# Optimization experiments

Hardware: AMD Instinct MI355X
Metric: run time of the kernel (lower is better)

Reference implementation:

```python
import jax, jax.numpy as jnp
import numpy as np

N = 20000       # nodes
E = 320000      # edges (without self-loops)
D_IN = 256
HID = 64        # per-head channels, layer 1
HEADS = 4
D_OUT = 256
EPS = 1e-5      # LayerNorm eps
SLOPE = 0.2     # LeakyReLU negative slope (PyG GATConv default)


def setup_inputs() -> dict:
    key = jax.random.key(0)
    ks = jax.random.split(key, 10)
    def glorot(k, shape):
        fan_in, fan_out = shape[0], int(np.prod(shape[1:]))
        s = np.sqrt(2.0 / (fan_in + fan_out)).astype(np.float32)
        return jax.random.normal(k, shape, dtype=jnp.float32) * s
    x = jax.random.normal(ks[0], (N, D_IN), dtype=jnp.float32)
    edge_index = jax.random.randint(ks[1], (2, E), 0, N, dtype=jnp.int64)
    return {
        "x": x,
        "edge_index": edge_index,
        # layer 1: GATConv(D_IN, HID, heads=4, concat=True)
        "W1": glorot(ks[2], (D_IN, HEADS * HID)),
        "a1_src": glorot(ks[3], (HEADS, HID)),
        "a1_dst": glorot(ks[4], (HEADS, HID)),
        "b1": jnp.zeros((HEADS * HID,), jnp.float32),
        # LayerNorm(HEADS*HID)
        "ln_g": jnp.ones((HEADS * HID,), jnp.float32),
        "ln_b": jnp.zeros((HEADS * HID,), jnp.float32),
        # layer 2: GATConv(HEADS*HID, D_OUT, heads=1, concat=False)
        "W2": glorot(ks[5], (HEADS * HID, D_OUT)),
        "a2_src": glorot(ks[6], (1, D_OUT)),
        "a2_dst": glorot(ks[7], (1, D_OUT)),
        "b2": jnp.zeros((D_OUT,), jnp.float32),
    }


def _gat(x, src, dst, W, a_src, a_dst, b, heads, ch, concat):
    """PyG-style GATConv (self-loops already appended to src/dst)."""
    n = x.shape[0]
    h = (x @ W).reshape(n, heads, ch)                      # [n,H,C]
    es = (h * a_src).sum(-1)                               # [n,H] src logits
    ed = (h * a_dst).sum(-1)                               # [n,H] dst logits
    e = jax.nn.leaky_relu(es[src] + ed[dst], SLOPE)        # [Etot,H]
    # softmax over incoming edges of each dst node (stable)
    m = jax.ops.segment_max(e, dst, num_segments=n)
    w = jnp.exp(e - m[dst])
    den = jax.ops.segment_sum(w, dst, num_segments=n)
    alpha = w / den[dst]                                   # [Etot,H]
    msg = h[src] * alpha[:, :, None]                       # [Etot,H,C]
    out = jax.ops.segment_sum(msg, dst, num_segments=n)    # [n,H,C]
    out = out.reshape(n, heads * ch) if concat else out.mean(axis=1)
    return out + b


def _layernorm(x, g, b):
    mu = x.mean(-1, keepdims=True)
    v = ((x - mu) ** 2).mean(-1, keepdims=True)
    return (x - mu) * jax.lax.rsqrt(v + EPS) * g + b


def reference(x, edge_index, W1, a1_src, a1_dst, b1, ln_g, ln_b, W2, a2_src, a2_dst, b2):
    loops = jnp.arange(N, dtype=edge_index.dtype)
    src = jnp.concatenate([edge_index[0], loops])
    dst = jnp.concatenate([edge_index[1], loops])
    h = _gat(x, src, dst, W1, a1_src, a1_dst, b1, HEADS, HID, True)
    h = jax.nn.relu(_layernorm(h, ln_g, ln_b))             # dropout is identity in eval
    out = _gat(h, src, dst, W2, a2_src, a2_dst, b2, 1, D_OUT, False)
    return out
```

## Files before the change

### kernel.cpp

```cpp
#include <hip/hip_runtime.h>
#include <hip/hip_bf16.h>
#include <math.h>

#define N_NODES 20000
#define N_EDGES 320000
#define N_ETOT  (N_EDGES + N_NODES)
#define SLOPE 0.2f
#define LN_EPS 1e-5f

typedef __attribute__((ext_vector_type(8))) short short8v;
typedef __attribute__((ext_vector_type(4))) float f32x4;

__device__ __forceinline__ float lrelu(float x) { return x > 0.f ? x : SLOPE * x; }

__device__ __forceinline__ float rlf(float v, int l) {
  return __uint_as_float(__builtin_amdgcn_readlane(__float_as_uint(v), l));
}
__device__ __forceinline__ int rli(int v, int l) { return __builtin_amdgcn_readlane(v, l); }

__device__ __forceinline__ unsigned short f2bf(float f) {
  __hip_bfloat16 h = __float2bfloat16(f);
  return *reinterpret_cast<unsigned short*>(&h);
}
__device__ __forceinline__ float bf2f(unsigned short u) {
  return __uint_as_float(((unsigned int)u) << 16);
}

__global__ __launch_bounds__(256) void k_count(const int* __restrict__ ei, int* __restrict__ cnt) {
  int i = blockIdx.x * 256 + threadIdx.x;
  if (i >= N_ETOT) return;
  int d = (i < N_EDGES) ? ei[N_EDGES + i] : (i - N_EDGES);
  atomicAdd(&cnt[d], 1);
}

__global__ __launch_bounds__(1024) void k_scan(int* __restrict__ cnt, int* __restrict__ off) {
  __shared__ int wsum[16], wpref[16];
  __shared__ int base_s;
  int tid = threadIdx.x, lane = tid & 63, wid = tid >> 6;
  if (tid == 0) { base_s = 0; off[0] = 0; }
  __syncthreads();
  for (int c = 0; c < 20; ++c) {
    int i = c * 1024 + tid;
    int v = (i < N_NODES) ? cnt[i] : 0;
    if (i < N_NODES) cnt[i] = 0;
    int incl = v;
#pragma unroll
    for (int d = 1; d < 64; d <<= 1) { int t = __shfl_up(incl, d); if (lane >= d) incl += t; }
    if (lane == 63) wsum[wid] = incl;
    __syncthreads();
    if (wid == 0 && lane < 16) {
      int s = wsum[lane];
#pragma unroll
      for (int d = 1; d < 16; d <<= 1) { int t = __shfl_up(s, d); if (lane >= d) s += t; }
      wpref[lane] = s;
    }
    __syncthreads();
    int wbase = wid ? wpref[wid - 1] : 0;
    if (i < N_NODES) off[i + 1] = base_s + wbase + incl;
    __syncthreads();
    if (tid == 0) base_s += wpref[15];
    __syncthreads();
  }
}

__global__ __launch_bounds__(256) void k_scatter(const int* __restrict__ ei, const int* __restrict__ off,
                                                 int* __restrict__ cursor, int* __restrict__ srcs) {
  int i = blockIdx.x * 256 + threadIdx.x;
  if (i >= N_ETOT) return;
  int s, d;
  if (i < N_EDGES) { s = ei[i]; d = ei[N_EDGES + i]; } else { s = i - N_EDGES; d = s; }
  int pos = off[d] + atomicAdd(&cursor[d], 1);
  srcs[pos] = s;
}

__global__ __launch_bounds__(256) void k_prep(const float* __restrict__ W1, const float* __restrict__ W2,
                                              unsigned short* __restrict__ P1, unsigned short* __restrict__ P2) {
  int b = blockIdx.x, t = threadIdx.x;
  int e = (b & 255) * 256 + t;
  int j = e & 7, lane = (e >> 3) & 63, nf = (e >> 9) & 7, ks = (e >> 12) & 7, nh = (e >> 15) & 1;
  int col = nh * 128 + nf * 16 + (lane & 15);
  int k = ks * 32 + (lane >> 4) * 8 + j;
  if (b < 256) P1[e] = f2bf(W1[k * 256 + col]);
  else         P2[e] = f2bf(W2[k * 256 + col]);
}

template <int A_BF16, int HEADS>
__global__ __launch_bounds__(256) void k_mfma_gemm(const void* __restrict__ Av,
                                                   const unsigned short* __restrict__ Wp,
                                                   const float* __restrict__ asrc,
                                                   const float* __restrict__ adst,
                                                   unsigned short* __restrict__ C,
                                                   float* __restrict__ es, float* __restrict__ ed) {
  int gwave = blockIdx.x * 4 + (threadIdx.x >> 6);
  int wtile = gwave >> 1;
  int nhalf = gwave & 1;
  int lane = threadIdx.x & 63;
  int r = lane & 15, kg = lane >> 4;
  int rbase = wtile * 16;
  int cbase = nhalf * 128;

  f32x4 acc[8];
#pragma unroll
  for (int i = 0; i < 8; ++i) acc[i] = (f32x4){0.f, 0.f, 0.f, 0.f};

  const float* Af = (const float*)Av;
  const unsigned short* Ab = (const unsigned short*)Av;
  const unsigned short* Wb = Wp + nhalf * 32768;

#pragma unroll
  for (int ks = 0; ks < 8; ++ks) {
    int koff = ks * 32 + kg * 8;
    short8v a;
    if (A_BF16) {
      int4 raw = *reinterpret_cast<const int4*>(&Ab[(size_t)(rbase + r) * 256 + koff]);
      a = __builtin_bit_cast(short8v, raw);
    } else {
      float4 lo = *reinterpret_cast<const float4*>(&Af[(size_t)(rbase + r) * 256 + koff]);
      float4 hi = *reinterpret_cast<const float4*>(&Af[(size_t)(rbase + r) * 256 + koff + 4]);
      a[0] = (short)f2bf(lo.x); a[1] = (short)f2bf(lo.y); a[2] = (short)f2bf(lo.z); a[3] = (short)f2bf(lo.w);
      a[4] = (short)f2bf(hi.x); a[5] = (short)f2bf(hi.y); a[6] = (short)f2bf(hi.z); a[7] = (short)f2bf(hi.w);
    }
#pragma unroll
    for (int nf = 0; nf < 8; ++nf) {
      int4 braw = *reinterpret_cast<const int4*>(&Wb[(size_t)(ks * 8 + nf) * 512 + lane * 8]);
      short8v b = __builtin_bit_cast(short8v, braw);
      acc[nf] = __builtin_amdgcn_mfma_f32_16x16x32_bf16(a, b, acc[nf], 0, 0, 0);
    }
  }

#pragma unroll
  for (int nf = 0; nf < 8; ++nf) {
#pragma unroll
    for (int q = 0; q < 4; ++q) {
      int row = rbase + kg * 4 + q;
      int col = cbase + nf * 16 + r;
      C[(size_t)row * 256 + col] = f2bf(acc[nf][q]);
    }
  }

  float as_v[8], ad_v[8];
#pragma unroll
  for (int nf = 0; nf < 8; ++nf) {
    int col = cbase + nf * 16 + r;
    as_v[nf] = asrc[col];
    ad_v[nf] = adst[col];
  }
  if (HEADS == 4) {
#pragma unroll
    for (int q = 0; q < 4; ++q) {
      float s0 = 0.f, s1 = 0.f, d0 = 0.f, d1 = 0.f;
#pragma unroll
      for (int nf = 0; nf < 4; ++nf) {
        s0 = fmaf(acc[nf][q], as_v[nf], s0);
        d0 = fmaf(acc[nf][q], ad_v[nf], d0);
        s1 = fmaf(acc[nf + 4][q], as_v[nf + 4], s1);
        d1 = fmaf(acc[nf + 4][q], ad_v[nf + 4], d1);
      }
#pragma unroll
      for (int s = 1; s < 16; s <<= 1) {
        s0 += __shfl_xor(s0, s); s1 += __shfl_xor(s1, s);
        d0 += __shfl_xor(d0, s); d1 += __shfl_xor(d1, s);
      }
      if (r == 0) {
        int row = rbase + kg * 4 + q;
        int hl = nhalf * 2;
        atomicAdd(&es[row * 4 + hl], s0);
        atomicAdd(&es[row * 4 + hl + 1], s1);
        atomicAdd(&ed[row * 4 + hl], d0);
        atomicAdd(&ed[row * 4 + hl + 1], d1);
      }
    }
  } else {
#pragma unroll
    for (int q = 0; q < 4; ++q) {
      float s0 = 0.f, d0 = 0.f;
#pragma unroll
      for (int nf = 0; nf < 8; ++nf) {
        s0 = fmaf(acc[nf][q], as_v[nf], s0);
        d0 = fmaf(acc[nf][q], ad_v[nf], d0);
      }
#pragma unroll
      for (int s = 1; s < 16; s <<= 1) {
        s0 += __shfl_xor(s0, s);
        d0 += __shfl_xor(d0, s);
      }
      if (r == 0) {
        int row = rbase + kg * 4 + q;
        atomicAdd(&es[row], s0);
        atomicAdd(&ed[row], d0);
      }
    }
  }
}

__global__ __launch_bounds__(256) void k_gat1_ln(const unsigned short* __restrict__ h1,
                                                 const float* __restrict__ es, const float* __restrict__ ed,
                                                 const int* __restrict__ off, const int* __restrict__ srcs,
                                                 const float* __restrict__ b1, const float* __restrict__ lng,
                                                 const float* __restrict__ lnb, unsigned short* __restrict__ hmid) {
  int n = (blockIdx.x * 256 + threadIdx.x) >> 6;
  if (n >= N_NODES) return;
  int lane = threadIdx.x & 63;
  int myh = lane >> 4;
  int beg = off[n], end = off[n + 1], deg = end - beg;
  float4 edv = *reinterpret_cast<const float4*>(&ed[n * 4]);
  float ax = 0.f, ay = 0.f, az = 0.f, aw = 0.f;
  float invden;

  if (deg <= 64) {
    int sv = 0;
    float e0 = -1e30f, e1 = -1e30f, e2 = -1e30f, e3 = -1e30f;
    bool valid = lane < deg;
    if (valid) {
      sv = srcs[beg + lane];
      float4 esv = *reinterpret_cast<const float4*>(&es[sv * 4]);
      e0 = lrelu(esv.x + edv.x); e1 = lrelu(esv.y + edv.y);
      e2 = lrelu(esv.z + edv.z); e3 = lrelu(esv.w + edv.w);
    }
    float m0 = e0, m1 = e1, m2 = e2, m3 = e3;
#pragma unroll
    for (int s = 1; s < 64; s <<= 1) {
      m0 = fmaxf(m0, __shfl_xor(m0, s)); m1 = fmaxf(m1, __shfl_xor(m1, s));
      m2 = fmaxf(m2, __shfl_xor(m2, s)); m3 = fmaxf(m3, __shfl_xor(m3, s));
    }
    float w0 = valid ? __expf(e0 - m0) : 0.f;
    float w1 = valid ? __expf(e1 - m1) : 0.f;
    float w2 = valid ? __expf(e2 - m2) : 0.f;
    float w3 = valid ? __expf(e3 - m3) : 0.f;
    float d0 = w0, d1 = w1, d2 = w2, d3 = w3;
#pragma unroll
    for (int s = 1; s < 64; s <<= 1) {
      d0 += __shfl_xor(d0, s); d1 += __shfl_xor(d1, s);
      d2 += __shfl_xor(d2, s); d3 += __shfl_xor(d3, s);
    }
    float den = (myh == 0) ? d0 : (myh == 1) ? d1 : (myh == 2) ? d2 : d3;
    invden = 1.f / den;

    int j = 0;
    for (; j + 4 <= deg; j += 4) {
      int s0 = rli(sv, j), s1 = rli(sv, j + 1), s2 = rli(sv, j + 2), s3 = rli(sv, j + 3);
      ushort4 v0 = *reinterpret_cast<const ushort4*>(&h1[(size_t)s0 * 256 + lane * 4]);
      ushort4 v1 = *reinterpret_cast<const ushort4*>(&h1[(size_t)s1 * 256 + lane * 4]);
      ushort4 v2 = *reinterpret_cast<const ushort4*>(&h1[(size_t)s2 * 256 + lane * 4]);
      ushort4 v3 = *reinterpret_cast<const ushort4*>(&h1[(size_t)s3 * 256 + lane * 4]);
#pragma unroll
      for (int q = 0; q < 4; ++q) {
        int jj = j + q;
        float w0j = rlf(w0, jj), w1j = rlf(w1, jj), w2j = rlf(w2, jj), w3j = rlf(w3, jj);
        float wj = (myh == 0) ? w0j : (myh == 1) ? w1j : (myh == 2) ? w2j : w3j;
        ushort4 v = (q == 0) ? v0 : (q == 1) ? v1 : (q == 2) ? v2 : v3;
        ax = fmaf(wj, bf2f(v.x), ax); ay = fmaf(wj, bf2f(v.y), ay);
        az = fmaf(wj, bf2f(v.z), az); aw = fmaf(wj, bf2f(v.w), aw);
      }
    }
    for (; j < deg; ++j) {
      int sj = rli(sv, j);
      float w0j = rlf(w0, j), w1j = rlf(w1, j), w2j = rlf(w2, j), w3j = rlf(w3, j);
      float wj = (myh == 0) ? w0j : (myh == 1) ? w1j : (myh == 2) ? w2j : w3j;
      ushort4 v = *reinterpret_cast<const ushort4*>(&h1[(size_t)sj * 256 + lane * 4]);
      ax = fmaf(wj, bf2f(v.x), ax); ay = fmaf(wj, bf2f(v.y), ay);
      az = fmaf(wj, bf2f(v.z), az); aw = fmaf(wj, bf2f(v.w), aw);
    }
  } else {
    float m0 = -1e30f, m1 = -1e30f, m2 = -1e30f, m3 = -1e30f;
    for (int j = beg + lane; j < end; j += 64) {
      int s = srcs[j];
      float4 esv = *reinterpret_cast<const float4*>(&es[s * 4]);
      m0 = fmaxf(m0, lrelu(esv.x + edv.x)); m1 = fmaxf(m1, lrelu(esv.y + edv.y));
      m2 = fmaxf(m2, lrelu(esv.z + edv.z)); m3 = fmaxf(m3, lrelu(esv.w + edv.w));
    }
#pragma unroll
    for (int s = 1; s < 64; s <<= 1) {
      m0 = fmaxf(m0, __shfl_xor(m0, s)); m1 = fmaxf(m1, __shfl_xor(m1, s));
      m2 = fmaxf(m2, __shfl_xor(m2, s)); m3 = fmaxf(m3, __shfl_xor(m3, s));
    }
    float edh = (myh == 0) ? edv.x : (myh == 1) ? edv.y : (myh == 2) ? edv.z : edv.w;
    float mh = (myh == 0) ? m0 : (myh == 1) ? m1 : (myh == 2) ? m2 : m3;
    float den = 0.f;
    for (int j = beg; j < end; ++j) {
      int s = srcs[j];
      float e = lrelu(es[s * 4 + myh] + edh);
      float w = __expf(e - mh);
      den += w;
      ushort4 v = *reinterpret_cast<const ushort4*>(&h1[(size_t)s * 256 + lane * 4]);
      ax = fmaf(w, bf2f(v.x), ax); ay = fmaf(w, bf2f(v.y), ay);
      az = fmaf(w, bf2f(v.z), az); aw = fmaf(w, bf2f(v.w), aw);
    }
    invden = 1.f / den;
  }

  float4 bb = *reinterpret_cast<const float4*>(&b1[lane * 4]);
  float vx = ax * invden + bb.x, vy = ay * invden + bb.y;
  float vz = az * invden + bb.z, vw = aw * invden + bb.w;
  float sum = vx + vy + vz + vw;
  float sq = vx * vx + vy * vy + vz * vz + vw * vw;
#pragma unroll
  for (int s = 1; s < 64; s <<= 1) { sum += __shfl_xor(sum, s); sq += __shfl_xor(sq, s); }
  float mu = sum * (1.f / 256.f);
  float var = sq * (1.f / 256.f) - mu * mu;
  float rstd = rsqrtf(var + LN_EPS);
  float4 g = *reinterpret_cast<const float4*>(&lng[lane * 4]);
  float4 lb = *reinterpret_cast<const float4*>(&lnb[lane * 4]);
  ushort4 o;
  o.x = f2bf(fmaxf(0.f, (vx - mu) * rstd * g.x + lb.x));
  o.y = f2bf(fmaxf(0.f, (vy - mu) * rstd * g.y + lb.y));
  o.z = f2bf(fmaxf(0.f, (vz - mu) * rstd * g.z + lb.z));
  o.w = f2bf(fmaxf(0.f, (vw - mu) * rstd * g.w + lb.w));
  *reinterpret_cast<ushort4*>(&hmid[(size_t)n * 256 + lane * 4]) = o;
}

__global__ __launch_bounds__(256) void k_gat2(const unsigned short* __restrict__ h2,
                                              const float* __restrict__ es, const float* __restrict__ ed,
                                              const int* __restrict__ off, const int* __restrict__ srcs,
                                              const float* __restrict__ b2, float* __restrict__ out) {
  int n = (blockIdx.x * 256 + threadIdx.x) >> 6;
  if (n >= N_NODES) return;
  int lane = threadIdx.x & 63;
  int beg = off[n], end = off[n + 1], deg = end - beg;
  float edn = ed[n];
  float ax = 0.f, ay = 0.f, az = 0.f, aw = 0.f;
  float invden;

  if (deg <= 64) {
    int sv = 0;
    float e = -1e30f;
    bool valid = lane < deg;
    if (valid) {
      sv = srcs[beg + lane];
      e = lrelu(es[sv] + edn);
    }
    float m = e;
#pragma unroll
    for (int s = 1; s < 64; s <<= 1) m = fmaxf(m, __shfl_xor(m, s));
    float wv = valid ? __expf(e - m) : 0.f;
    float den = wv;
#pragma unroll
    for (int s = 1; s < 64; s <<= 1) den += __shfl_xor(den, s);
    invden = 1.f / den;

    int j = 0;
    for (; j + 4 <= deg; j += 4) {
      int s0 = rli(sv, j), s1 = rli(sv, j + 1), s2 = rli(sv, j + 2), s3 = rli(sv, j + 3);
      ushort4 v0 = *reinterpret_cast<const ushort4*>(&h2[(size_t)s0 * 256 + lane * 4]);
      ushort4 v1 = *reinterpret_cast<const ushort4*>(&h2[(size_t)s1 * 256 + lane * 4]);
      ushort4 v2 = *reinterpret_cast<const ushort4*>(&h2[(size_t)s2 * 256 + lane * 4]);
      ushort4 v3 = *reinterpret_cast<const ushort4*>(&h2[(size_t)s3 * 256 + lane * 4]);
      float wj0 = rlf(wv, j), wj1 = rlf(wv, j + 1), wj2 = rlf(wv, j + 2), wj3 = rlf(wv, j + 3);
      ax = fmaf(wj0, bf2f(v0.x), ax); ay = fmaf(wj0, bf2f(v0.y), ay);
      az = fmaf(wj0, bf2f(v0.z), az); aw = fmaf(wj0, bf2f(v0.w), aw);
      ax = fmaf(wj1, bf2f(v1.x), ax); ay = fmaf(wj1, bf2f(v1.y), ay);
      az = fmaf(wj1, bf2f(v1.z), az); aw = fmaf(wj1, bf2f(v1.w), aw);
      ax = fmaf(wj2, bf2f(v2.x), ax); ay = fmaf(wj2, bf2f(v2.y), ay);
      az = fmaf(wj2, bf2f(v2.z), az); aw = fmaf(wj2, bf2f(v2.w), aw);
      ax = fmaf(wj3, bf2f(v3.x), ax); ay = fmaf(wj3, bf2f(v3.y), ay);
      az = fmaf(wj3, bf2f(v3.z), az); aw = fmaf(wj3, bf2f(v3.w), aw);
    }
    for (; j < deg; ++j) {
      int sj = rli(sv, j);
      float wj = rlf(wv, j);
      ushort4 v = *reinterpret_cast<const ushort4*>(&h2[(size_t)sj * 256 + lane * 4]);
      ax = fmaf(wj, bf2f(v.x), ax); ay = fmaf(wj, bf2f(v.y), ay);
      az = fmaf(wj, bf2f(v.z), az); aw = fmaf(wj, bf2f(v.w), aw);
    }
  } else {
    float m = -1e30f;
    for (int j = beg + lane; j < end; j += 64) m = fmaxf(m, lrelu(es[srcs[j]] + edn));
#pragma unroll
    for (int s = 1; s < 64; s <<= 1) m = fmaxf(m, __shfl_xor(m, s));
    float den = 0.f;
    for (int j = beg; j < end; ++j) {
      int s = srcs[j];
      float w = __expf(lrelu(es[s] + edn) - m);
      den += w;
      ushort4 v = *reinterpret_cast<const ushort4*>(&h2[(size_t)s * 256 + lane * 4]);
      ax = fmaf(w, bf2f(v.x), ax); ay = fmaf(w, bf2f(v.y), ay);
      az = fmaf(w, bf2f(v.z), az); aw = fmaf(w, bf2f(v.w), aw);
    }
    invden = 1.f / den;
  }

  float4 bb = *reinterpret_cast<const float4*>(&b2[lane * 4]);
  float4 o = make_float4(ax * invden + bb.x, ay * invden + bb.y, az * invden + bb.z, aw * invden + bb.w);
  *reinterpret_cast<float4*>(&out[(size_t)n * 256 + lane * 4]) = o;
}

extern "C" void kernel_launch(void* const* d_in, const int* in_sizes, int n_in,
                              void* d_out, int out_size, void* d_ws, size_t ws_size,
                              hipStream_t stream) {
  (void)in_sizes; (void)n_in; (void)out_size; (void)ws_size;
  const float* x   = (const float*)d_in[0];
  const int*   ei  = (const int*)d_in[1];
  const float* W1  = (const float*)d_in[2];
  const float* a1s = (const float*)d_in[3];
  const float* a1d = (const float*)d_in[4];
  const float* b1  = (const float*)d_in[5];
  const float* lng = (const float*)d_in[6];
  const float* lnb = (const float*)d_in[7];
  const float* W2  = (const float*)d_in[8];
  const float* a2s = (const float*)d_in[9];
  const float* a2d = (const float*)d_in[10];
  const float* b2  = (const float*)d_in[11];
  float* out = (float*)d_out;

  char* ws = (char*)d_ws;
  unsigned short* h1b   = (unsigned short*)(ws + 0);
  unsigned short* hmidb = (unsigned short*)(ws + 10240000);
  unsigned short* h2b   = (unsigned short*)(ws + 20480000);
  unsigned short* Wp1   = (unsigned short*)(ws + 30720000);
  unsigned short* Wp2   = (unsigned short*)(ws + 30851072);
  float* es1 = (float*)(ws + 30982144);
  float* ed1 = (float*)(ws + 31302144);
  float* es2 = (float*)(ws + 31622144);
  float* ed2 = (float*)(ws + 31702144);
  int*   off = (int*)(ws + 31782144);
  int*   cnt = (int*)(ws + 31862148);
  int*   srcs = (int*)(ws + 31942148);

  hipMemsetAsync(cnt, 0, N_NODES * sizeof(int), stream);
  hipMemsetAsync(es1, 0, 800000, stream);

  k_count<<<(N_ETOT + 255) / 256, 256, 0, stream>>>(ei, cnt);
  k_scan<<<1, 1024, 0, stream>>>(cnt, off);
  k_scatter<<<(N_ETOT + 255) / 256, 256, 0, stream>>>(ei, off, cnt, srcs);

  k_prep<<<512, 256, 0, stream>>>(W1, W2, Wp1, Wp2);

  k_mfma_gemm<0, 4><<<625, 256, 0, stream>>>((const void*)x, Wp1, a1s, a1d, h1b, es1, ed1);
  k_gat1_ln<<<(N_NODES * 64) / 256, 256, 0, stream>>>(h1b, es1, ed1, off, srcs, b1, lng, lnb, hmidb);

  k_mfma_gemm<1, 1><<<625, 256, 0, stream>>>((const void*)hmidb, Wp2, a2s, a2d, h2b, es2, ed2);
  k_gat2<<<(N_NODES * 64) / 256, 256, 0, stream>>>(h2b, es2, ed2, off, srcs, b2, out);
}
```

Baseline: 232.8 us.

## Fuse CSR build and weight packing into one persistent kernel with grid barriers

Replaces the two memsets and the count, single-block scan, scatter and weight-prep kernels with one 256-block persistent kernel that uses atomic grid-wide barriers between phases. The scan becomes a two-level multi-block scan instead of a serial 1024-thread loop. The goal is to cut launch overhead and the slow single-block scan. In exchange it relies on all 256 blocks being co-resident for the spin barrier, and it keeps a small memset to reset the barrier counter.

```diff
diff --git a/kernel.cpp b/kernel.cpp
--- a/kernel.cpp
+++ b/kernel.cpp
@@ -7,6 +7,8 @@
 #define N_ETOT  (N_EDGES + N_NODES)
 #define SLOPE 0.2f
 #define LN_EPS 1e-5f
+#define NBLK 256
+#define NTHR 65536
 
 typedef __attribute__((ext_vector_type(8))) short short8v;
 typedef __attribute__((ext_vector_type(4))) float f32x4;
@@ -26,62 +28,102 @@
   return __uint_as_float(((unsigned int)u) << 16);
 }
 
-__global__ __launch_bounds__(256) void k_count(const int* __restrict__ ei, int* __restrict__ cnt) {
-  int i = blockIdx.x * 256 + threadIdx.x;
-  if (i >= N_ETOT) return;
-  int d = (i < N_EDGES) ? ei[N_EDGES + i] : (i - N_EDGES);
-  atomicAdd(&cnt[d], 1);
-}
-
-__global__ __launch_bounds__(1024) void k_scan(int* __restrict__ cnt, int* __restrict__ off) {
-  __shared__ int wsum[16], wpref[16];
-  __shared__ int base_s;
-  int tid = threadIdx.x, lane = tid & 63, wid = tid >> 6;
-  if (tid == 0) { base_s = 0; off[0] = 0; }
+__device__ __forceinline__ int aload(const int* p) {
+  return __hip_atomic_load(p, __ATOMIC_RELAXED, __HIP_MEMORY_SCOPE_AGENT);
+}
+__device__ __forceinline__ void astore(int* p, int v) {
+  __hip_atomic_store(p, v, __ATOMIC_RELAXED, __HIP_MEMORY_SCOPE_AGENT);
+}
+
+__device__ __forceinline__ void gbar(unsigned* bar, unsigned target) {
+  __threadfence();
   __syncthreads();
-  for (int c = 0; c < 20; ++c) {
-    int i = c * 1024 + tid;
-    int v = (i < N_NODES) ? cnt[i] : 0;
-    if (i < N_NODES) cnt[i] = 0;
-    int incl = v;
-#pragma unroll
-    for (int d = 1; d < 64; d <<= 1) { int t = __shfl_up(incl, d); if (lane >= d) incl += t; }
-    if (lane == 63) wsum[wid] = incl;
-    __syncthreads();
-    if (wid == 0 && lane < 16) {
-      int s = wsum[lane];
-#pragma unroll
-      for (int d = 1; d < 16; d <<= 1) { int t = __shfl_up(s, d); if (lane >= d) s += t; }
-      wpref[lane] = s;
-    }
-    __syncthreads();
-    int wbase = wid ? wpref[wid - 1] : 0;
-    if (i < N_NODES) off[i + 1] = base_s + wbase + incl;
-    __syncthreads();
-    if (tid == 0) base_s += wpref[15];
-    __syncthreads();
-  }
-}
-
-__global__ __launch_bounds__(256) void k_scatter(const int* __restrict__ ei, const int* __restrict__ off,
-                                                 int* __restrict__ cursor, int* __restrict__ srcs) {
-  int i = blockIdx.x * 256 + threadIdx.x;
-  if (i >= N_ETOT) return;
-  int s, d;
-  if (i < N_EDGES) { s = ei[i]; d = ei[N_EDGES + i]; } else { s = i - N_EDGES; d = s; }
-  int pos = off[d] + atomicAdd(&cursor[d], 1);
-  srcs[pos] = s;
-}
-
-__global__ __launch_bounds__(256) void k_prep(const float* __restrict__ W1, const float* __restrict__ W2,
-                                              unsigned short* __restrict__ P1, unsigned short* __restrict__ P2) {
-  int b = blockIdx.x, t = threadIdx.x;
-  int e = (b & 255) * 256 + t;
-  int j = e & 7, lane = (e >> 3) & 63, nf = (e >> 9) & 7, ks = (e >> 12) & 7, nh = (e >> 15) & 1;
-  int col = nh * 128 + nf * 16 + (lane & 15);
-  int k = ks * 32 + (lane >> 4) * 8 + j;
-  if (b < 256) P1[e] = f2bf(W1[k * 256 + col]);
-  else         P2[e] = f2bf(W2[k * 256 + col]);
+  if (threadIdx.x == 0) {
+    __hip_atomic_fetch_add(bar, 1u, __ATOMIC_RELEASE, __HIP_MEMORY_SCOPE_AGENT);
+    while (__hip_atomic_load(bar, __ATOMIC_ACQUIRE, __HIP_MEMORY_SCOPE_AGENT) < target)
+      __builtin_amdgcn_s_sleep(4);
+  }
+  __syncthreads();
+  __threadfence();
+}
+
+__device__ __forceinline__ int blockScan(int val, int tid, int* ldsw, int* total) {
+  int lane = tid & 63, w = tid >> 6;
+  int incl = val;
+#pragma unroll
+  for (int d = 1; d < 64; d <<= 1) { int t = __shfl_up(incl, d); if (lane >= d) incl += t; }
+  if (lane == 63) ldsw[w] = incl;
+  __syncthreads();
+  if (w == 0 && lane < 4) {
+    int s = ldsw[lane];
+#pragma unroll
+    for (int d = 1; d < 4; d <<= 1) { int t = __shfl_up(s, d); if (lane >= d) s += t; }
+    ldsw[lane] = s;
+  }
+  __syncthreads();
+  if (w > 0) incl += ldsw[w - 1];
+  *total = ldsw[3];
+  return incl;
+}
+
+__global__ __launch_bounds__(256) void k_graph(const int* __restrict__ ei,
+                                               const float* __restrict__ W1, const float* __restrict__ W2,
+                                               unsigned short* __restrict__ P1w, unsigned short* __restrict__ P2w,
+                                               int* __restrict__ cnt, int* __restrict__ off,
+                                               int* __restrict__ srcs, float* __restrict__ eszero,
+                                               int* __restrict__ bsum, unsigned* __restrict__ bar) {
+  __shared__ int ldsw[4];
+  int tid = threadIdx.x;
+  int b = blockIdx.x;
+  int g = b * 256 + tid;
+
+  if (g < N_NODES) cnt[g] = 0;
+  {
+    float4* z = (float4*)eszero;
+    if (g < 50000) z[g] = make_float4(0.f, 0.f, 0.f, 0.f);
+    int e = g;
+    int j = e & 7, lane = (e >> 3) & 63, nf = (e >> 9) & 7, ks = (e >> 12) & 7, nh = (e >> 15) & 1;
+    int col = nh * 128 + nf * 16 + (lane & 15);
+    int k = ks * 32 + (lane >> 4) * 8 + j;
+    P1w[e] = f2bf(W1[k * 256 + col]);
+    P2w[e] = f2bf(W2[k * 256 + col]);
+  }
+  gbar(bar, 256u);
+
+  for (int i = g; i < N_ETOT; i += NTHR) {
+    int d = (i < N_EDGES) ? ei[N_EDGES + i] : (i - N_EDGES);
+    atomicAdd(&cnt[d], 1);
+  }
+  gbar(bar, 512u);
+
+  int val = (g < N_NODES) ? aload(&cnt[g]) : 0;
+  int tot;
+  int incl = blockScan(val, tid, ldsw, &tot);
+  if (tid == 0) astore(&bsum[b], tot);
+  gbar(bar, 768u);
+
+  if (b == 0) {
+    int v = aload(&bsum[tid]);
+    int t2;
+    int inc2 = blockScan(v, tid, ldsw, &t2);
+    astore(&bsum[tid], inc2);
+  }
+  gbar(bar, 1024u);
+
+  int base = b ? aload(&bsum[b - 1]) : 0;
+  if (g < N_NODES) {
+    off[g + 1] = base + incl;
+    astore(&cnt[g], 0);
+  }
+  if (g == 0) off[0] = 0;
+  gbar(bar, 1280u);
+
+  for (int i = g; i < N_ETOT; i += NTHR) {
+    int s, d;
+    if (i < N_EDGES) { s = ei[i]; d = ei[N_EDGES + i]; } else { s = i - N_EDGES; d = s; }
+    int pos = aload(&off[d]) + atomicAdd(&cnt[d], 1);
+    srcs[pos] = s;
+  }
 }
 
 template <int A_BF16, int HEADS>
@@ -415,15 +457,12 @@
   int*   off = (int*)(ws + 31782144);
   int*   cnt = (int*)(ws + 31862148);
   int*   srcs = (int*)(ws + 31942148);
-
-  hipMemsetAsync(cnt, 0, N_NODES * sizeof(int), stream);
-  hipMemsetAsync(es1, 0, 800000, stream);
-
-  k_count<<<(N_ETOT + 255) / 256, 256, 0, stream>>>(ei, cnt);
-  k_scan<<<1, 1024, 0, stream>>>(cnt, off);
-  k_scatter<<<(N_ETOT + 255) / 256, 256, 0, stream>>>(ei, off, cnt, srcs);
-
-  k_prep<<<512, 256, 0, stream>>>(W1, W2, Wp1, Wp2);
+  unsigned* bar = (unsigned*)(ws + 33302148);
+  int*   bsum = (int*)(ws + 33302160);
+
+  hipMemsetAsync(bar, 0, 8, stream);
+
+  k_graph<<<NBLK, 256, 0, stream>>>(ei, W1, W2, Wp1, Wp2, cnt, off, srcs, es1, bsum, bar);
 
   k_mfma_gemm<0, 4><<<625, 256, 0, stream>>>((const void*)x, Wp1, a1s, a1d, h1b, es1, ed1);
   k_gat1_ln<<<(N_NODES * 64) / 256, 256, 0, stream>>>(h1b, es1, ed1, off, srcs, b1, lng, lnb, hmidb);
```

New measurement: 419.0 us. +80.0%, slower.

## Parallelize CSR scan, fuse count with weight prep, widen GEMM waves to full rows

Applied to the files above, without the earlier changes.

The single-block serial scan over 20 chunks becomes a two-kernel multi-block scan: per-block scan, then an add of the block-sum prefix. Edge counting and weight packing are merged into one launch, and the memset for es1/ed1 is dropped. Each GEMM wave now covers all 256 output columns for its 16 rows, so attention logits are written directly instead of combined with float atomics across two column halves. This cuts launch count, serialization and atomics, but doubles accumulator registers per wave and halves the number of waves, which may lower occupancy.

```diff
diff --git a/kernel.cpp b/kernel.cpp
--- a/kernel.cpp
+++ b/kernel.cpp
@@ -7,6 +7,7 @@
 #define N_ETOT  (N_EDGES + N_NODES)
 #define SLOPE 0.2f
 #define LN_EPS 1e-5f
+#define CNT_BLOCKS 1329
 
 typedef __attribute__((ext_vector_type(8))) short short8v;
 typedef __attribute__((ext_vector_type(4))) float f32x4;
@@ -26,41 +27,77 @@
   return __uint_as_float(((unsigned int)u) << 16);
 }
 
-__global__ __launch_bounds__(256) void k_count(const int* __restrict__ ei, int* __restrict__ cnt) {
-  int i = blockIdx.x * 256 + threadIdx.x;
-  if (i >= N_ETOT) return;
-  int d = (i < N_EDGES) ? ei[N_EDGES + i] : (i - N_EDGES);
-  atomicAdd(&cnt[d], 1);
-}
-
-__global__ __launch_bounds__(1024) void k_scan(int* __restrict__ cnt, int* __restrict__ off) {
-  __shared__ int wsum[16], wpref[16];
-  __shared__ int base_s;
-  int tid = threadIdx.x, lane = tid & 63, wid = tid >> 6;
-  if (tid == 0) { base_s = 0; off[0] = 0; }
+__global__ __launch_bounds__(256) void k_count_prep(const int* __restrict__ ei, int* __restrict__ cnt,
+                                                    const float* __restrict__ W1, const float* __restrict__ W2,
+                                                    unsigned short* __restrict__ P1, unsigned short* __restrict__ P2) {
+  int b = blockIdx.x, tid = threadIdx.x;
+  if (b < CNT_BLOCKS) {
+    int i = b * 256 + tid;
+    if (i < N_ETOT) {
+      int d = (i < N_EDGES) ? ei[N_EDGES + i] : (i - N_EDGES);
+      atomicAdd(&cnt[d], 1);
+    }
+  } else {
+    int e = (b - CNT_BLOCKS) * 256 + tid;
+    int j = e & 7, lane = (e >> 3) & 63, nf = (e >> 9) & 15, ks = (e >> 13) & 7;
+    int col = nf * 16 + (lane & 15);
+    int k = ks * 32 + (lane >> 4) * 8 + j;
+    P1[e] = f2bf(W1[k * 256 + col]);
+    P2[e] = f2bf(W2[k * 256 + col]);
+  }
+}
+
+__device__ __forceinline__ int blockScan512(int val, int tid, int* ldsw, int* total) {
+  int lane = tid & 63, w = tid >> 6;
+  int incl = val;
+#pragma unroll
+  for (int d = 1; d < 64; d <<= 1) { int t = __shfl_up(incl, d); if (lane >= d) incl += t; }
+  if (lane == 63) ldsw[w] = incl;
   __syncthreads();
-  for (int c = 0; c < 20; ++c) {
-    int i = c * 1024 + tid;
-    int v = (i < N_NODES) ? cnt[i] : 0;
-    if (i < N_NODES) cnt[i] = 0;
-    int incl = v;
-#pragma unroll
-    for (int d = 1; d < 64; d <<= 1) { int t = __shfl_up(incl, d); if (lane >= d) incl += t; }
-    if (lane == 63) wsum[wid] = incl;
-    __syncthreads();
-    if (wid == 0 && lane < 16) {
-      int s = wsum[lane];
-#pragma unroll
-      for (int d = 1; d < 16; d <<= 1) { int t = __shfl_up(s, d); if (lane >= d) s += t; }
-      wpref[lane] = s;
-    }
-    __syncthreads();
-    int wbase = wid ? wpref[wid - 1] : 0;
-    if (i < N_NODES) off[i + 1] = base_s + wbase + incl;
-    __syncthreads();
-    if (tid == 0) base_s += wpref[15];
-    __syncthreads();
-  }
+  if (w == 0 && lane < 8) {
+    int s = ldsw[lane];
+#pragma unroll
+    for (int d = 1; d < 8; d <<= 1) { int t = __shfl_up(s, d); if (lane >= d) s += t; }
+    ldsw[lane] = s;
+  }
+  __syncthreads();
+  if (w > 0) incl += ldsw[w - 1];
+  *total = ldsw[7];
+  return incl;
+}
+
+__global__ __launch_bounds__(512) void k_scanA(const int* __restrict__ cnt, int* __restrict__ off,
+                                               int* __restrict__ bsum) {
+  __shared__ int ldsw[8];
+  int tid = threadIdx.x, b = blockIdx.x;
+  int g = b * 512 + tid;
+  int val = (g < N_NODES) ? cnt[g] : 0;
+  int tot;
+  int incl = blockScan512(val, tid, ldsw, &tot);
+  if (g < N_NODES) off[g + 1] = incl;
+  if (tid == 0) bsum[b] = tot;
+}
+
+__global__ __launch_bounds__(512) void k_scanB(int* __restrict__ off, const int* __restrict__ bsum,
+                                               int* __restrict__ cnt) {
+  __shared__ int sbase;
+  int tid = threadIdx.x, b = blockIdx.x;
+  if (tid < 64) {
+    int v = (tid < 40) ? bsum[tid] : 0;
+    int inc = v;
+#pragma unroll
+    for (int d = 1; d < 64; d <<= 1) { int t = __shfl_up(inc, d); if (tid >= d) inc += t; }
+    int base = (b == 0) ? 0 : rli(inc, b - 1);
+    if (tid == 0) sbase = base;
+  }
+  __syncthreads();
+  int base = sbase;
+  int g = b * 512 + tid;
+  if (g < N_NODES) {
+    off[g + 1] += base;
+    cnt[g] = 0;
+  }
+  if (g == 0) off[0] = 0;
 }
 
 __global__ __launch_bounds__(256) void k_scatter(const int* __restrict__ ei, const int* __restrict__ off,
@@ -73,39 +110,25 @@
   srcs[pos] = s;
 }
 
-__global__ __launch_bounds__(256) void k_prep(const float* __restrict__ W1, const float* __restrict__ W2,
-                                              unsigned short* __restrict__ P1, unsigned short* __restrict__ P2) {
-  int b = blockIdx.x, t = threadIdx.x;
-  int e = (b & 255) * 256 + t;
-  int j = e & 7, lane = (e >> 3) & 63, nf = (e >> 9) & 7, ks = (e >> 12) & 7, nh = (e >> 15) & 1;
-  int col = nh * 128 + nf * 16 + (lane & 15);
-  int k = ks * 32 + (lane >> 4) * 8 + j;
-  if (b < 256) P1[e] = f2bf(W1[k * 256 + col]);
-  else         P2[e] = f2bf(W2[k * 256 + col]);
-}
-
 template <int A_BF16, int HEADS>
-__global__ __launch_bounds__(256) void k_mfma_gemm(const void* __restrict__ Av,
-                                                   const unsigned short* __restrict__ Wp,
-                                                   const float* __restrict__ asrc,
-                                                   const float* __restrict__ adst,
-                                                   unsigned short* __restrict__ C,
-                                                   float* __restrict__ es, float* __restrict__ ed) {
+__global__ __launch_bounds__(256) void k_gemm(const void* __restrict__ Av,
+                                              const unsigned short* __restrict__ Wp,
+                                              const float* __restrict__ asrc,
+                                              const float* __restrict__ adst,
+                                              unsigned short* __restrict__ C,
+                                              float* __restrict__ es, float* __restrict__ ed) {
   int gwave = blockIdx.x * 4 + (threadIdx.x >> 6);
-  int wtile = gwave >> 1;
-  int nhalf = gwave & 1;
+  if (gwave >= 1250) return;
   int lane = threadIdx.x & 63;
   int r = lane & 15, kg = lane >> 4;
-  int rbase = wtile * 16;
-  int cbase = nhalf * 128;
-
-  f32x4 acc[8];
-#pragma unroll
-  for (int i = 0; i < 8; ++i) acc[i] = (f32x4){0.f, 0.f, 0.f, 0.f};
+  int rbase = gwave * 16;
+
+  f32x4 acc[16];
+#pragma unroll
+  for (int i = 0; i < 16; ++i) acc[i] = (f32x4){0.f, 0.f, 0.f, 0.f};
 
   const float* Af = (const float*)Av;
   const unsigned short* Ab = (const unsigned short*)Av;
-  const unsigned short* Wb = Wp + nhalf * 32768;
 
 #pragma unroll
   for (int ks = 0; ks < 8; ++ks) {
@@ -121,53 +144,53 @@
       a[4] = (short)f2bf(hi.x); a[5] = (short)f2bf(hi.y); a[6] = (short)f2bf(hi.z); a[7] = (short)f2bf(hi.w);
     }
 #pragma unroll
-    for (int nf = 0; nf < 8; ++nf) {
-      int4 braw = *reinterpret_cast<const int4*>(&Wb[(size_t)(ks * 8 + nf) * 512 + lane * 8]);
-      short8v b = __builtin_bit_cast(short8v, braw);
-      acc[nf] = __builtin_amdgcn_mfma_f32_16x16x32_bf16(a, b, acc[nf], 0, 0, 0);
-    }
-  }
-
-#pragma unroll
-  for (int nf = 0; nf < 8; ++nf) {
+    for (int nf = 0; nf < 16; ++nf) {
+      int4 braw = *reinterpret_cast<const int4*>(&Wp[(size_t)(ks * 16 + nf) * 512 + lane * 8]);
+      short8v bfr = __builtin_bit_cast(short8v, braw);
+      acc[nf] = __builtin_amdgcn_mfma_f32_16x16x32_bf16(a, bfr, acc[nf], 0, 0, 0);
+    }
+  }
+
+#pragma unroll
+  for (int nf = 0; nf < 16; ++nf) {
 #pragma unroll
     for (int q = 0; q < 4; ++q) {
-      int row = rbase + kg * 4 + q;
-      int col = cbase + nf * 16 + r;
-      C[(size_t)row * 256 + col] = f2bf(acc[nf][q]);
-    }
-  }
-
-  float as_v[8], ad_v[8];
-#pragma unroll
-  for (int nf = 0; nf < 8; ++nf) {
-    int col = cbase + nf * 16 + r;
-    as_v[nf] = asrc[col];
-    ad_v[nf] = adst[col];
+      C[(size_t)(rbase + kg * 4 + q) * 256 + nf * 16 + r] = f2bf(acc[nf][q]);
+    }
+  }
+
+  float as_v[16], ad_v[16];
+#pragma unroll
+  for (int nf = 0; nf < 16; ++nf) {
+    as_v[nf] = asrc[nf * 16 + r];
+    ad_v[nf] = adst[nf * 16 + r];
   }
   if (HEADS == 4) {
 #pragma unroll
     for (int q = 0; q < 4; ++q) {
-      float s0 = 0.f, s1 = 0.f, d0 = 0.f, d1 = 0.f;
-#pragma unroll
-      for (int nf = 0; nf < 4; ++nf) {
-        s0 = fmaf(acc[nf][q], as_v[nf], s0);
-        d0 = fmaf(acc[nf][q], ad_v[nf], d0);
-        s1 = fmaf(acc[nf + 4][q], as_v[nf + 4], s1);
-        d1 = fmaf(acc[nf + 4][q], ad_v[nf + 4], d1);
-      }
-#pragma unroll
-      for (int s = 1; s < 16; s <<= 1) {
-        s0 += __shfl_xor(s0, s); s1 += __shfl_xor(s1, s);
-        d0 += __shfl_xor(d0, s); d1 += __shfl_xor(d1, s);
+      float hs[4], hd[4];
+#pragma unroll
+      for (int h = 0; h < 4; ++h) {
+        hs[h] = 0.f; hd[h] = 0.f;
+#pragma unroll
+        for (int t = 0; t < 4; ++t) {
+          int nf = h * 4 + t;
+          hs[h] = fmaf(acc[nf][q], as_v[nf], hs[h]);
+          hd[h] = fmaf(acc[nf][q], ad_v[nf], hd[h]);
+        }
+#pragma unroll
+        for (int s = 1; s < 16; s <<= 1) {
+          hs[h] += __shfl_xor(hs[h], s);
+          hd[h] += __shfl_xor(hd[h], s);
+        }
       }
       if (r == 0) {
         int row = rbase + kg * 4 + q;
-        int hl = nhalf * 2;
-        atomicAdd(&es[row * 4 + hl], s0);
-        atomicAdd(&es[row * 4 + hl + 1], s1);
-        atomicAdd(&ed[row * 4 + hl], d0);
-        atomicAdd(&ed[row * 4 + hl + 1], d1);
+#pragma unroll
+        for (int h = 0; h < 4; ++h) {
+          es[row * 4 + h] = hs[h];
+          ed[row * 4 + h] = hd[h];
+        }
       }
     }
   } else {
@@ -175,7 +198,7 @@
     for (int q = 0; q < 4; ++q) {
       float s0 = 0.f, d0 = 0.f;
 #pragma unroll
-      for (int nf = 0; nf < 8; ++nf) {
+      for (int nf = 0; nf < 16; ++nf) {
         s0 = fmaf(acc[nf][q], as_v[nf], s0);
         d0 = fmaf(acc[nf][q], ad_v[nf], d0);
       }
@@ -186,8 +209,8 @@
       }
       if (r == 0) {
         int row = rbase + kg * 4 + q;
-        atomicAdd(&es[row], s0);
-        atomicAdd(&ed[row], d0);
+        es[row] = s0;
+        ed[row] = d0;
       }
     }
   }
@@ -415,19 +438,17 @@
   int*   off = (int*)(ws + 31782144);
   int*   cnt = (int*)(ws + 31862148);
   int*   srcs = (int*)(ws + 31942148);
+  int*   bsum = (int*)(ws + 33302160);
 
   hipMemsetAsync(cnt, 0, N_NODES * sizeof(int), stream);
-  hipMemsetAsync(es1, 0, 800000, stream);
-
-  k_count<<<(N_ETOT + 255) / 256, 256, 0, stream>>>(ei, cnt);
-  k_scan<<<1, 1024, 0, stream>>>(cnt, off);
-  k_scatter<<<(N_ETOT + 255) / 256, 256, 0, stream>>>(ei, off, cnt, srcs);
-
-  k_prep<<<512, 256, 0, stream>>>(W1, W2, Wp1, Wp2);
-
-  k_mfma_gemm<0, 4><<<625, 256, 0, stream>>>((const void*)x, Wp1, a1s, a1d, h1b, es1, ed1);
+  k_count_prep<<<CNT_BLOCKS + 256, 256, 0, stream>>>(ei, cnt, W1, W2, Wp1, Wp2);
+  k_scanA<<<40, 512, 0, stream>>>(cnt, off, bsum);
+  k_scanB<<<40, 512, 0, stream>>>(off, bsum, cnt);
+  k_scatter<<<CNT_BLOCKS, 256, 0, stream>>>(ei, off, cnt, srcs);
+
+  k_gemm<0, 4><<<313, 256, 0, stream>>>((const void*)x, Wp1, a1s, a1d, h1b, es1, ed1);
   k_gat1_ln<<<(N_NODES * 64) / 256, 256, 0, stream>>>(h1b, es1, ed1, off, srcs, b1, lng, lnb, hmidb);
 
-  k_mfma_gemm<1, 1><<<625, 256, 0, stream>>>((const void*)hmidb, Wp2, a2s, a2d, h2b, es2, ed2);
+  k_gemm<1, 1><<<313, 256, 0, stream>>>((const void*)hmidb, Wp2, a2s, a2d, h2b, es2, ed2);
   k_gat2<<<(N_NODES * 64) / 256, 256, 0, stream>>>(h2b, es2, ed2, off, srcs, b2, out);
 }
```

Result: faster. 217.3 us (-6.6%).
